# Kernel tuning notes

Measured on AMD Instinct MI355X. Metric: run time of the kernel, lower is better.

Reference implementation:

```python
import jax, jax.numpy as jnp
import numpy as np

NUM_HEADS = 16


def setup_inputs() -> dict:
    key = jax.random.key(0)
    ks = jax.random.split(key, 7)
    E = 1024
    s = 0.02
    return {
        "x": jax.random.normal(ks[0], (2, 2048, E), dtype=jnp.float32),
        "Wq": jax.random.normal(ks[1], (E, E), dtype=jnp.float32) * s,
        "bq": jax.random.normal(ks[2], (E,), dtype=jnp.float32) * s,
        "Wk": jax.random.normal(ks[3], (E, E), dtype=jnp.float32) * s,
        "bk": jax.random.normal(ks[4], (E,), dtype=jnp.float32) * s,
        "Wv": jax.random.normal(ks[5], (E, E), dtype=jnp.float32) * s,
        "bv": jax.random.normal(ks[6], (E,), dtype=jnp.float32) * s,
    }


def reference(x, Wq, bq, Wk, bk, Wv, bv):
    b, s, e = x.shape
    h = NUM_HEADS
    d = e // h  # head_dim = 64
    # nn.Linear: y = x @ W^T + b
    q = x @ Wq.T + bq
    k = x @ Wk.T + bk
    v = x @ Wv.T + bv
    # Faithful reshape chain from the source: (b,s,e)->(b,s,h,d)->(-1,s,d)
    # (raw reshape, NO transpose, matching the original buggy layout)
    q = q.reshape(b, s, h, d).reshape(-1, s, d)
    k = k.reshape(b, s, h, d).reshape(-1, s, d)
    v = v.reshape(b, s, h, d).reshape(-1, s, d)
    # Scaled scores; note the source returns qk @ v (softmax result discarded)
    scale = 1.0 / np.sqrt(d).astype(np.float32)
    qk = jnp.einsum('bqd,bkd->bqk', q, k) * scale  # [b*h, s, s]
    out = jnp.einsum('bqk,bkd->bqd', qk, v)        # [b*h, s, d]
    return out
```

## Files before the change

kernel.cpp:

```cpp
#include <hip/hip_runtime.h>
#include <hip/hip_bf16.h>


#define E_DIM 1024
#define N_ROWS 4096

typedef __attribute__((ext_vector_type(8))) short bf16x8;
typedef __attribute__((ext_vector_type(4))) float f32x4;

#define QB_U 0
#define KB_U 4194304
#define VB_U 8388608
#define XB_U 12582912
#define WB_U 16777216
#define P_F  9961472
#define TB_U 24117248

__device__ __forceinline__ unsigned short f2b(float f) {
    union { float f; unsigned int i; } c; c.f = f;
    unsigned int r = c.i + 0x7FFFu + ((c.i >> 16) & 1u);
    return (unsigned short)(r >> 16);
}

typedef __attribute__((address_space(1))) const void* gptr_t;
typedef __attribute__((address_space(3))) void* lptr_t;
__device__ __forceinline__ void gl_lds16(const void* g, void* l) {
    __builtin_amdgcn_global_load_lds((gptr_t)g, (lptr_t)l, 16, 0, 0);
}

__global__ __launch_bounds__(256) void cvt_bf16(
    const float* __restrict__ x,  const float* __restrict__ wq,
    const float* __restrict__ wk, const float* __restrict__ wv,
    unsigned short* __restrict__ dst0)
{
    const int seg = blockIdx.y;
    const float* __restrict__ src;
    unsigned short* __restrict__ dst;
    if (seg < 4) { src = x + (size_t)seg * 1048576; dst = dst0 + (size_t)seg * 1048576; }
    else {
        src = (seg == 4) ? wq : (seg == 5) ? wk : wv;
        dst = dst0 + 4194304 + (size_t)(seg - 4) * 1048576;
    }
    const int i = blockIdx.x * 256 + threadIdx.x;
    const float4 a = *(const float4*)(src + (size_t)i * 8);
    const float4 b = *(const float4*)(src + (size_t)i * 8 + 4);
    uint4 o;
    o.x = (unsigned)f2b(a.x) | ((unsigned)f2b(a.y) << 16);
    o.y = (unsigned)f2b(a.z) | ((unsigned)f2b(a.w) << 16);
    o.z = (unsigned)f2b(b.x) | ((unsigned)f2b(b.y) << 16);
    o.w = (unsigned)f2b(b.z) | ((unsigned)f2b(b.w) << 16);
    *(uint4*)(dst + (size_t)i * 8) = o;
}

__global__ __launch_bounds__(256, 3) void qkv_gemm_mfma(
    const unsigned short* __restrict__ Xb,
    const unsigned short* __restrict__ Wb,
    const float* __restrict__ bq, const float* __restrict__ bk,
    const float* __restrict__ bv,
    unsigned short* __restrict__ qkv)
{
    const int which = blockIdx.z;
    const unsigned short* __restrict__ W = Wb + (size_t)which * (1024 * 1024);
    const float* __restrict__ bias = (which == 0) ? bq : (which == 1) ? bk : bv;
    unsigned short* __restrict__ Y = qkv + (size_t)which * ((size_t)N_ROWS * E_DIM);

    __shared__ __align__(16) unsigned short Als[128 * 32];
    __shared__ __align__(16) unsigned short Bls[128 * 32];

    const int tid  = threadIdx.x;
    const int w    = tid >> 6;
    const int lane = tid & 63;
    const int m0 = blockIdx.x * 128;
    const int n0 = blockIdx.y * 128;
    const int wm = (w >> 1) * 64;
    const int wn = (w & 1) * 64;

    f32x4 acc[4][4];
    #pragma unroll
    for (int i = 0; i < 4; ++i)
        #pragma unroll
        for (int j = 0; j < 4; ++j)
            acc[i][j] = f32x4{0.f, 0.f, 0.f, 0.f};

    const int srow = w * 32 + (lane >> 2);
    const int skc  = ((lane & 3) ^ ((lane >> 3) & 3)) * 8;
    const int quad = lane >> 4;
    const int fm   = lane & 15;
    const int sw2  = (fm >> 1) & 3;

    for (int k0 = 0; k0 < E_DIM; k0 += 32) {
        gl_lds16((const void*)(Xb + (size_t)(m0 + srow) * E_DIM + k0 + skc),
                 (void*)((char*)Als + (w * 2 + 0) * 1024));
        gl_lds16((const void*)(Xb + (size_t)(m0 + srow + 16) * E_DIM + k0 + skc),
                 (void*)((char*)Als + (w * 2 + 1) * 1024));
        gl_lds16((const void*)(W + (size_t)(n0 + srow) * E_DIM + k0 + skc),
                 (void*)((char*)Bls + (w * 2 + 0) * 1024));
        gl_lds16((const void*)(W + (size_t)(n0 + srow + 16) * E_DIM + k0 + skc),
                 (void*)((char*)Bls + (w * 2 + 1) * 1024));
        __syncthreads();

        const int slot = (quad ^ sw2) * 8;
        bf16x8 af[4], bf[4];
        #pragma unroll
        for (int t = 0; t < 4; ++t) {
            af[t] = *(const bf16x8*)(Als + (wm + t * 16 + fm) * 32 + slot);
            bf[t] = *(const bf16x8*)(Bls + (wn + t * 16 + fm) * 32 + slot);
        }
        #pragma unroll
        for (int rt = 0; rt < 4; ++rt)
            #pragma unroll
            for (int ct = 0; ct < 4; ++ct)
                acc[rt][ct] = __builtin_amdgcn_mfma_f32_16x16x32_bf16(
                    af[rt], bf[ct], acc[rt][ct], 0, 0, 0);
        __syncthreads();
    }

    float bcol[4];
    #pragma unroll
    for (int ct = 0; ct < 4; ++ct) bcol[ct] = bias[n0 + wn + ct * 16 + fm];

    const int rbase = (lane >> 4) * 4;
    #pragma unroll
    for (int rt = 0; rt < 4; ++rt) {
        #pragma unroll
        for (int ct = 0; ct < 4; ++ct) {
            #pragma unroll
            for (int r = 0; r < 4; ++r) {
                const int row = m0 + wm + rt * 16 + rbase + r;
                const int col = n0 + wn + ct * 16 + fm;
                Y[(size_t)row * E_DIM + col] = f2b(acc[rt][ct][r] + bcol[ct]);
            }
        }
    }
}

__device__ __forceinline__ int sw_idx(int row, int r) {
    return row * 64 + (((((r) >> 3) & 7) ^ (row & 7)) << 3) + (r & 7);
}

__global__ __launch_bounds__(256) void kT_mfma(
    const unsigned short* __restrict__ qkv, float* __restrict__ P)
{
    const size_t base = (size_t)blockIdx.x * (2048 * 64) + (size_t)blockIdx.y * (256 * 64);
    const unsigned short* __restrict__ Kb = qkv + KB_U + base;
    const unsigned short* __restrict__ Vb = qkv + VB_U + base;
    float* __restrict__ Pout = P + ((size_t)blockIdx.x * 8 + blockIdx.y) * 4096;

    __shared__ __align__(16) unsigned short Kt[64 * 64];
    __shared__ __align__(16) unsigned short Vt[64 * 64];

    const int tid  = threadIdx.x;
    const int w    = tid >> 6;
    const int lane = tid & 63;
    const int rl   = tid & 63;
    const int eo   = (tid >> 6) * 16;
    const int quad = lane >> 4;
    const int fm   = lane & 15;
    const int sw8  = fm & 7;

    f32x4 acc[4];
    #pragma unroll
    for (int nt = 0; nt < 4; ++nt) acc[nt] = f32x4{0.f, 0.f, 0.f, 0.f};

    for (int rb = 0; rb < 256; rb += 64) {
        union { uint4 u; unsigned short s[8]; } k0, k1, v0, v1;
        const size_t ga = (size_t)(rb + rl) * 64 + eo;
        k0.u = *(const uint4*)(Kb + ga);
        k1.u = *(const uint4*)(Kb + ga + 8);
        v0.u = *(const uint4*)(Vb + ga);
        v1.u = *(const uint4*)(Vb + ga + 8);
        __syncthreads();
        #pragma unroll
        for (int j = 0; j < 8; ++j) {
            Kt[sw_idx(eo + j, rl)]     = k0.s[j];
            Kt[sw_idx(eo + 8 + j, rl)] = k1.s[j];
            Vt[sw_idx(eo + j, rl)]     = v0.s[j];
            Vt[sw_idx(eo + 8 + j, rl)] = v1.s[j];
        }
        __syncthreads();
        #pragma unroll
        for (int kk = 0; kk < 2; ++kk) {
            const int slot = ((kk * 4 + quad) ^ sw8) << 3;
            const bf16x8 af = *(const bf16x8*)(Vt + (w * 16 + fm) * 64 + slot);
            #pragma unroll
            for (int nt = 0; nt < 4; ++nt) {
                const bf16x8 bf = *(const bf16x8*)(Kt + (nt * 16 + fm) * 64 + slot);
                acc[nt] = __builtin_amdgcn_mfma_f32_16x16x32_bf16(af, bf, acc[nt], 0, 0, 0);
            }
        }
    }

    const int rbase = (lane >> 4) * 4;
    #pragma unroll
    for (int nt = 0; nt < 4; ++nt)
        #pragma unroll
        for (int r = 0; r < 4; ++r)
            Pout[(size_t)(w * 16 + rbase + r) * 64 + nt * 16 + fm] = acc[nt][r];
}

__global__ __launch_bounds__(256) void reduce_T(
    const float* __restrict__ P, unsigned short* __restrict__ TB)
{
    const int idx = blockIdx.x * 256 + threadIdx.x;
    const int i   = idx >> 12;
    const int off = idx & 4095;
    const float* p = P + (size_t)i * 8 * 4096 + off;
    float s = 0.0f;
    #pragma unroll
    for (int c = 0; c < 8; ++c) s += p[(size_t)c * 4096];
    TB[(size_t)i * 4096 + off] = f2b(s);
}

__global__ __launch_bounds__(256, 2) void qT_mfma(
    const unsigned short* __restrict__ qkv,
    const unsigned short* __restrict__ TB,
    float* __restrict__ out)
{
    __shared__ __align__(16) unsigned short Als[128 * 64];
    __shared__ __align__(16) unsigned short Bls[64 * 64];

    const int bx   = blockIdx.x;
    const int r0   = bx * 128;
    const int i    = bx >> 4;
    const int tid  = threadIdx.x;
    const int w    = tid >> 6;
    const int lane = tid & 63;
    const int quad = lane >> 4;
    const int fm   = lane & 15;
    const int sw8  = fm & 7;

    const unsigned short* __restrict__ Qb = qkv + QB_U + (size_t)r0 * 64;
    const unsigned short* __restrict__ Tb = TB + (size_t)i * 4096;

    const int soff = (lane >> 3) * 64 + (((lane & 7) ^ ((lane >> 3) & 7)) << 3);
    #pragma unroll
    for (int c = 0; c < 4; ++c)
        gl_lds16((const void*)(Qb + (w * 4 + c) * 512 + soff),
                 (void*)((char*)Als + (w * 4 + c) * 1024));
    #pragma unroll
    for (int c = 0; c < 2; ++c)
        gl_lds16((const void*)(Tb + (w * 2 + c) * 512 + soff),
                 (void*)((char*)Bls + (w * 2 + c) * 1024));
    __syncthreads();

    bf16x8 af[2][2], bf[4][2];
    #pragma unroll
    for (int mt = 0; mt < 2; ++mt)
        #pragma unroll
        for (int kk = 0; kk < 2; ++kk)
            af[mt][kk] = *(const bf16x8*)(Als + (w * 32 + mt * 16 + fm) * 64
                                          + (((kk * 4 + quad) ^ sw8) << 3));
    #pragma unroll
    for (int nt = 0; nt < 4; ++nt)
        #pragma unroll
        for (int kk = 0; kk < 2; ++kk)
            bf[nt][kk] = *(const bf16x8*)(Bls + (nt * 16 + fm) * 64
                                          + (((kk * 4 + quad) ^ sw8) << 3));

    f32x4 acc[2][4];
    #pragma unroll
    for (int mt = 0; mt < 2; ++mt)
        #pragma unroll
        for (int nt = 0; nt < 4; ++nt)
            acc[mt][nt] = f32x4{0.f, 0.f, 0.f, 0.f};

    #pragma unroll
    for (int kk = 0; kk < 2; ++kk)
        #pragma unroll
        for (int mt = 0; mt < 2; ++mt)
            #pragma unroll
            for (int nt = 0; nt < 4; ++nt)
                acc[mt][nt] = __builtin_amdgcn_mfma_f32_16x16x32_bf16(
                    af[mt][kk], bf[nt][kk], acc[mt][nt], 0, 0, 0);

    const int rbase = (lane >> 4) * 4;
    #pragma unroll
    for (int mt = 0; mt < 2; ++mt) {
        #pragma unroll
        for (int nt = 0; nt < 4; ++nt) {
            #pragma unroll
            for (int r = 0; r < 4; ++r) {
                const int row = r0 + w * 32 + mt * 16 + rbase + r;
                const int col = nt * 16 + fm;
                out[(size_t)row * 64 + col] = 0.125f * acc[mt][nt][r];
            }
        }
    }
}

extern "C" void kernel_launch(void* const* d_in, const int* in_sizes, int n_in,
                              void* d_out, int out_size, void* d_ws, size_t ws_size,
                              hipStream_t stream)
{
    const float* x  = (const float*)d_in[0];
    const float* Wq = (const float*)d_in[1];
    const float* bq = (const float*)d_in[2];
    const float* Wk = (const float*)d_in[3];
    const float* bk = (const float*)d_in[4];
    const float* Wv = (const float*)d_in[5];
    const float* bv = (const float*)d_in[6];
    float* wsf = (float*)d_ws;
    unsigned short* wsu = (unsigned short*)d_ws;
    float* out = (float*)d_out;

    dim3 gCvt(512, 7);
    cvt_bf16<<<gCvt, 256, 0, stream>>>(x, Wq, Wk, Wv, wsu + XB_U);

    dim3 gA(N_ROWS / 128, E_DIM / 128, 3);
    qkv_gemm_mfma<<<gA, 256, 0, stream>>>(wsu + XB_U, wsu + WB_U,
                                          bq, bk, bv, wsu + QB_U);

    dim3 gB(32, 8);
    kT_mfma<<<gB, 256, 0, stream>>>(wsu, wsf + P_F);

    reduce_T<<<512, 256, 0, stream>>>(wsf + P_F, wsu + TB_U);

    qT_mfma<<<512, 256, 0, stream>>>(wsu, wsu + TB_U, out);
}
```

Baseline: 130.1 us.

## Replace partial-sum reduce kernel with atomic accumulation and fuse bf16 conversion into consumer

Removes the separate reduce_T kernel. The split-K partial products of K^T V are now accumulated directly into an fp32 buffer with atomicAdd, and the buffer is zeroed by an extra grid slice of the conversion kernel. The kT kernel grid doubles to 16 chunks of 128 rows each. qT_mfma now loads the fp32 T and converts it to bf16 into swizzled LDS itself, which drops one launch and one round trip through global memory. In exchange it adds atomic contention (16 blocks per output tile) and makes the summation order nondeterministic.

```diff
diff --git a/kernel.cpp b/kernel.cpp
--- a/kernel.cpp
+++ b/kernel.cpp
@@ -14,7 +14,6 @@
 #define XB_U 12582912
 #define WB_U 16777216
 #define P_F  9961472
-#define TB_U 24117248
 
 __device__ __forceinline__ unsigned short f2b(float f) {
     union { float f; unsigned int i; } c; c.f = f;
@@ -31,9 +30,13 @@
 __global__ __launch_bounds__(256) void cvt_bf16(
     const float* __restrict__ x,  const float* __restrict__ wq,
     const float* __restrict__ wk, const float* __restrict__ wv,
-    unsigned short* __restrict__ dst0)
+    unsigned short* __restrict__ dst0, float* __restrict__ Tzero)
 {
     const int seg = blockIdx.y;
+    if (seg == 7) {
+        Tzero[blockIdx.x * 256 + threadIdx.x] = 0.0f;
+        return;
+    }
     const float* __restrict__ src;
     unsigned short* __restrict__ dst;
     if (seg < 4) { src = x + (size_t)seg * 1048576; dst = dst0 + (size_t)seg * 1048576; }
@@ -139,12 +142,12 @@
 }
 
 __global__ __launch_bounds__(256) void kT_mfma(
-    const unsigned short* __restrict__ qkv, float* __restrict__ P)
-{
-    const size_t base = (size_t)blockIdx.x * (2048 * 64) + (size_t)blockIdx.y * (256 * 64);
+    const unsigned short* __restrict__ qkv, float* __restrict__ TF)
+{
+    const size_t base = (size_t)blockIdx.x * (2048 * 64) + (size_t)blockIdx.y * (128 * 64);
     const unsigned short* __restrict__ Kb = qkv + KB_U + base;
     const unsigned short* __restrict__ Vb = qkv + VB_U + base;
-    float* __restrict__ Pout = P + ((size_t)blockIdx.x * 8 + blockIdx.y) * 4096;
+    float* __restrict__ Tf = TF + (size_t)blockIdx.x * 4096;
 
     __shared__ __align__(16) unsigned short Kt[64 * 64];
     __shared__ __align__(16) unsigned short Vt[64 * 64];
@@ -162,7 +165,7 @@
     #pragma unroll
     for (int nt = 0; nt < 4; ++nt) acc[nt] = f32x4{0.f, 0.f, 0.f, 0.f};
 
-    for (int rb = 0; rb < 256; rb += 64) {
+    for (int rb = 0; rb < 128; rb += 64) {
         union { uint4 u; unsigned short s[8]; } k0, k1, v0, v1;
         const size_t ga = (size_t)(rb + rl) * 64 + eo;
         k0.u = *(const uint4*)(Kb + ga);
@@ -195,25 +198,13 @@
     for (int nt = 0; nt < 4; ++nt)
         #pragma unroll
         for (int r = 0; r < 4; ++r)
-            Pout[(size_t)(w * 16 + rbase + r) * 64 + nt * 16 + fm] = acc[nt][r];
-}
-
-__global__ __launch_bounds__(256) void reduce_T(
-    const float* __restrict__ P, unsigned short* __restrict__ TB)
-{
-    const int idx = blockIdx.x * 256 + threadIdx.x;
-    const int i   = idx >> 12;
-    const int off = idx & 4095;
-    const float* p = P + (size_t)i * 8 * 4096 + off;
-    float s = 0.0f;
-    #pragma unroll
-    for (int c = 0; c < 8; ++c) s += p[(size_t)c * 4096];
-    TB[(size_t)i * 4096 + off] = f2b(s);
+            atomicAdd(&Tf[(size_t)(w * 16 + rbase + r) * 64 + nt * 16 + fm],
+                      acc[nt][r]);
 }
 
 __global__ __launch_bounds__(256, 2) void qT_mfma(
     const unsigned short* __restrict__ qkv,
-    const unsigned short* __restrict__ TB,
+    const float* __restrict__ TF,
     float* __restrict__ out)
 {
     __shared__ __align__(16) unsigned short Als[128 * 64];
@@ -230,17 +221,30 @@
     const int sw8  = fm & 7;
 
     const unsigned short* __restrict__ Qb = qkv + QB_U + (size_t)r0 * 64;
-    const unsigned short* __restrict__ Tb = TB + (size_t)i * 4096;
+    const float* __restrict__ Tf = TF + (size_t)i * 4096;
 
     const int soff = (lane >> 3) * 64 + (((lane & 7) ^ ((lane >> 3) & 7)) << 3);
     #pragma unroll
     for (int c = 0; c < 4; ++c)
         gl_lds16((const void*)(Qb + (w * 4 + c) * 512 + soff),
                  (void*)((char*)Als + (w * 4 + c) * 1024));
-    #pragma unroll
-    for (int c = 0; c < 2; ++c)
-        gl_lds16((const void*)(Tb + (w * 2 + c) * 512 + soff),
-                 (void*)((char*)Bls + (w * 2 + c) * 1024));
+
+    {
+        const int d  = tid >> 2;
+        const int e0 = (tid & 3) * 16;
+        float tv[16];
+        #pragma unroll
+        for (int j = 0; j < 4; ++j)
+            *(float4*)&tv[j * 4] = *(const float4*)(Tf + d * 64 + e0 + j * 4);
+        #pragma unroll
+        for (int s = 0; s < 2; ++s) {
+            union { uint4 u; unsigned short h[8]; } pk;
+            #pragma unroll
+            for (int j = 0; j < 8; ++j) pk.h[j] = f2b(tv[s * 8 + j]);
+            const int slot = (e0 >> 3) + s;
+            *(uint4*)(Bls + d * 64 + ((slot ^ (d & 7)) << 3)) = pk.u;
+        }
+    }
     __syncthreads();
 
     bf16x8 af[2][2], bf[4][2];
@@ -303,17 +307,15 @@
     unsigned short* wsu = (unsigned short*)d_ws;
     float* out = (float*)d_out;
 
-    dim3 gCvt(512, 7);
-    cvt_bf16<<<gCvt, 256, 0, stream>>>(x, Wq, Wk, Wv, wsu + XB_U);
+    dim3 gCvt(512, 8);
+    cvt_bf16<<<gCvt, 256, 0, stream>>>(x, Wq, Wk, Wv, wsu + XB_U, wsf + P_F);
 
     dim3 gA(N_ROWS / 128, E_DIM / 128, 3);
     qkv_gemm_mfma<<<gA, 256, 0, stream>>>(wsu + XB_U, wsu + WB_U,
                                           bq, bk, bv, wsu + QB_U);
 
-    dim3 gB(32, 8);
+    dim3 gB(32, 16);
     kT_mfma<<<gB, 256, 0, stream>>>(wsu, wsf + P_F);
 
-    reduce_T<<<512, 256, 0, stream>>>(wsf + P_F, wsu + TB_U);
-
-    qT_mfma<<<512, 256, 0, stream>>>(wsu, wsu + TB_U, out);
-}
+    qT_mfma<<<512, 256, 0, stream>>>(wsu, wsf + P_F, out);
+}
```

Result: slower. 132.8 us (+2.1%).
